# Performance work log

Hardware: AMD Instinct MI355X
Metric: run time of the kernel (lower is better)

## Reference

```python
import jax, jax.numpy as jnp
import numpy as np

EPS = 1e-5

def _ln(x, g, b):
    mu = jnp.mean(x, axis=-1, keepdims=True)
    var = jnp.mean(jnp.square(x - mu), axis=-1, keepdims=True)
    return (x - mu) * jax.lax.rsqrt(var + EPS) * g + b

def _gelu_new(x):
    # GPT-2 'gelu_new' (tanh approximation)
    c = jnp.asarray(np.sqrt(2.0 / np.pi), x.dtype)
    return 0.5 * x * (1.0 + jnp.tanh(c * (x + 0.044715 * x * x * x)))

def setup_inputs() -> dict:
    key = jax.random.key(0)
    ks = jax.random.split(key, 8)
    B, H, NH, HD, S = 16, 2048, 16, 128, 4096
    inv = lambda n: 1.0 / np.sqrt(n)
    return {
        "hidden_states": jax.random.normal(ks[0], (B, 1, H), jnp.float32),
        "cached_k": jax.random.normal(ks[1], (B, NH, S, HD), jnp.float32),
        "cached_v": jax.random.normal(ks[2], (B, NH, S, HD), jnp.float32),
        "ln1_g": jnp.ones((H,), jnp.float32),
        "ln1_b": jnp.zeros((H,), jnp.float32),
        "W_qkv": jax.random.normal(ks[3], (H, 3 * H), jnp.float32) * inv(H),
        "b_qkv": jnp.zeros((3 * H,), jnp.float32),
        "W_proj": jax.random.normal(ks[4], (H, H), jnp.float32) * inv(H),
        "b_proj": jnp.zeros((H,), jnp.float32),
        "ln2_g": jnp.ones((H,), jnp.float32),
        "ln2_b": jnp.zeros((H,), jnp.float32),
        "W_fc": jax.random.normal(ks[5], (H, 4 * H), jnp.float32) * inv(H),
        "b_fc": jnp.zeros((4 * H,), jnp.float32),
        "W_out": jax.random.normal(ks[6], (4 * H, H), jnp.float32) * inv(4 * H),
        "b_out": jnp.zeros((H,), jnp.float32),
    }

def reference(hidden_states, cached_k, cached_v, ln1_g, ln1_b, W_qkv, b_qkv,
              W_proj, b_proj, ln2_g, ln2_b, W_fc, b_fc, W_out, b_out):
    B, T, H = hidden_states.shape  # T == 1 (decode step)
    NH, HD = cached_k.shape[1], cached_k.shape[3]
    residual = hidden_states
    x = _ln(hidden_states, ln1_g, ln1_b)
    qkv = x @ W_qkv + b_qkv                        # [B,1,3H]
    q, k, v = jnp.split(qkv, 3, axis=-1)
    split = lambda t: t.reshape(B, T, NH, HD).transpose(0, 2, 1, 3)  # [B,NH,T,HD]
    q, k, v = split(q), split(k), split(v)
    k_full = jnp.concatenate([cached_k, k], axis=2)  # [B,NH,S+1,HD]
    v_full = jnp.concatenate([cached_v, v], axis=2)
    scale = 1.0 / jnp.sqrt(jnp.asarray(HD, q.dtype))
    scores = jnp.einsum('bhqd,bhkd->bhqk', q, k_full) * scale
    probs = jax.nn.softmax(scores, axis=-1)
    attn = jnp.einsum('bhqk,bhkd->bhqd', probs, v_full)  # [B,NH,1,HD]
    attn = attn.transpose(0, 2, 1, 3).reshape(B, T, H)
    attn = attn @ W_proj + b_proj
    h = attn + residual
    residual = h
    y = _ln(h, ln2_g, ln2_b)
    y = _gelu_new(y @ W_fc + b_fc) @ W_out + b_out
    return residual + y
```

## Files before the change

kernel.cpp:

```cpp
#include <hip/hip_runtime.h>
#include <hip/hip_bf16.h>

typedef unsigned int uint;


__global__ __launch_bounds__(256) void ln_f32_kernel(const float* __restrict__ in,
    const float* __restrict__ g, const float* __restrict__ bb, float* __restrict__ out)
{
    int row = blockIdx.x, t = threadIdx.x;
    const float* rp = in + row*2048;
    float4 a = ((const float4*)rp)[2*t];
    float4 b = ((const float4*)rp)[2*t+1];
    float v[8] = {a.x,a.y,a.z,a.w,b.x,b.y,b.z,b.w};
    float s=0.f, s2=0.f;
    #pragma unroll
    for(int i=0;i<8;i++){ s+=v[i]; s2+=v[i]*v[i]; }
    #pragma unroll
    for(int o=32;o>0;o>>=1){ s += __shfl_xor(s,o); s2 += __shfl_xor(s2,o); }
    __shared__ float red[8];
    int wv=t>>6, ln=t&63;
    if(ln==0){ red[wv]=s; red[4+wv]=s2; }
    __syncthreads();
    s  = red[0]+red[1]+red[2]+red[3];
    s2 = red[4]+red[5]+red[6]+red[7];
    float mu = s*(1.f/2048.f);
    float var = s2*(1.f/2048.f) - mu*mu;
    float rs = rsqrtf(var + 1e-5f);
    float4 g0 = ((const float4*)g)[2*t],  g1 = ((const float4*)g)[2*t+1];
    float4 b0 = ((const float4*)bb)[2*t], b1 = ((const float4*)bb)[2*t+1];
    float* op = out + row*2048 + t*8;
    float4 o0 = make_float4((v[0]-mu)*rs*g0.x+b0.x, (v[1]-mu)*rs*g0.y+b0.y,
                            (v[2]-mu)*rs*g0.z+b0.z, (v[3]-mu)*rs*g0.w+b0.w);
    float4 o1 = make_float4((v[4]-mu)*rs*g1.x+b1.x, (v[5]-mu)*rs*g1.y+b1.y,
                            (v[6]-mu)*rs*g1.z+b1.z, (v[7]-mu)*rs*g1.w+b1.w);
    ((float4*)op)[0]=o0; ((float4*)op)[1]=o1;
}

template<int KCHUNK>
__global__ __launch_bounds__(256) void gemm_sk(const float* __restrict__ X,
    const float* __restrict__ W, float* __restrict__ part, int K, int N, int colchunks)
{
    __shared__ float XS[16][KCHUNK];
    int cc = blockIdx.x % colchunks;
    int kc = blockIdx.x / colchunks;
    int k0 = kc * KCHUNK;
    for (int idx = threadIdx.x; idx < 16*KCHUNK; idx += 256){
        int m = idx / KCHUNK, i = idx % KCHUNK;
        XS[m][i] = X[m*K + k0 + i];
    }
    __syncthreads();
    int n0 = cc*512 + threadIdx.x*2;
    float a0[16], a1[16];
    #pragma unroll
    for(int m=0;m<16;m++){ a0[m]=0.f; a1[m]=0.f; }
    const float* Wp = W + (size_t)k0*N + n0;
    for (int i=0;i<KCHUNK;i+=4){
        float2 w0 = *(const float2*)(Wp + (size_t)(i+0)*N);
        float2 w1 = *(const float2*)(Wp + (size_t)(i+1)*N);
        float2 w2 = *(const float2*)(Wp + (size_t)(i+2)*N);
        float2 w3 = *(const float2*)(Wp + (size_t)(i+3)*N);
        #pragma unroll
        for(int m=0;m<16;m++){
            float4 x4 = *(const float4*)&XS[m][i];
            a0[m] += x4.x*w0.x + x4.y*w1.x + x4.z*w2.x + x4.w*w3.x;
            a1[m] += x4.x*w0.y + x4.y*w1.y + x4.z*w2.y + x4.w*w3.y;
        }
    }
    #pragma unroll
    for(int m=0;m<16;m++){
        *(float2*)&part[((size_t)(kc*16+m))*N + n0] = make_float2(a0[m], a1[m]);
    }
}

__global__ __launch_bounds__(256) void reduce_sk(const float* __restrict__ part, int N, int splitk,
    const float* __restrict__ bias, const float* __restrict__ res,
    float* __restrict__ outf, int mode)
{
    int n = blockIdx.x*256 + threadIdx.x;
    int m = blockIdx.y;
    size_t stride = (size_t)16*N;
    const float* p = part + (size_t)m*N + n;
    float s = 0.f;
    for (int kc=0;kc<splitk;kc++) s += p[(size_t)kc*stride];
    s += bias[n];
    if (mode==1 || mode==3) s += res[m*N+n];
    if (mode==2){
        float x = s;
        float t = tanhf(0.7978845608028654f*(x + 0.044715f*x*x*x));
        s = 0.5f*x*(1.f+t);
    }
    outf[m*N+n] = s;
}

__global__ __launch_bounds__(256, 8) void attn_chunk(const float* __restrict__ qkv,
    const float* __restrict__ Kc, const float* __restrict__ Vc, float* __restrict__ part)
{
    int h = blockIdx.y, b = blockIdx.z;
    int wave = threadIdx.x >> 6, lane = threadIdx.x & 63;
    int wc = blockIdx.x*4 + wave;
    int grp = lane >> 4, cl = lane & 15;
    const float* qrow = qkv + b*6144 + h*128 + cl*8;
    float4 qa = *(const float4*)qrow;
    float4 qb = *(const float4*)(qrow + 4);
    size_t bh = (size_t)(b*16+h);
    const float* Kbase = Kc + bh*4096*128;
    const float* Vbase = Vc + bh*4096*128;
    int jstart = wc * 128;
    float m = -1e30f, l = 0.f;
    float o[8];
    #pragma unroll
    for(int i=0;i<8;i++) o[i]=0.f;
    #pragma unroll 2
    for (int it=0; it<32; ++it){
        size_t off = (size_t)(jstart + it*4 + grp)*128 + cl*8;
        float4 ka = *(const float4*)(Kbase + off);
        float4 kb = *(const float4*)(Kbase + off + 4);
        float4 va = *(const float4*)(Vbase + off);
        float4 vb = *(const float4*)(Vbase + off + 4);
        float p = qa.x*ka.x + qa.y*ka.y + qa.z*ka.z + qa.w*ka.w
                + qb.x*kb.x + qb.y*kb.y + qb.z*kb.z + qb.w*kb.w;
        p += __shfl_xor(p,1); p += __shfl_xor(p,2);
        p += __shfl_xor(p,4); p += __shfl_xor(p,8);
        float sc = p * 0.08838834764831845f;
        float t = fmaxf(sc, __shfl_xor(sc,16));
        t = fmaxf(t, __shfl_xor(t,32));
        float mn = fmaxf(m, t);
        float f = __expf(m - mn);
        float e = __expf(sc - mn);
        l = l*f + e;
        o[0]=o[0]*f + e*va.x; o[1]=o[1]*f + e*va.y;
        o[2]=o[2]*f + e*va.z; o[3]=o[3]*f + e*va.w;
        o[4]=o[4]*f + e*vb.x; o[5]=o[5]*f + e*vb.y;
        o[6]=o[6]*f + e*vb.z; o[7]=o[7]*f + e*vb.w;
        m = mn;
    }
    if (wc == 31){
        const float* kn = qkv + b*6144 + 2048 + h*128 + cl*8;
        const float* vn = qkv + b*6144 + 4096 + h*128 + cl*8;
        float4 ka = *(const float4*)kn, kb = *(const float4*)(kn+4);
        float4 va = *(const float4*)vn, vb = *(const float4*)(vn+4);
        float p = qa.x*ka.x + qa.y*ka.y + qa.z*ka.z + qa.w*ka.w
                + qb.x*kb.x + qb.y*kb.y + qb.z*kb.z + qb.w*kb.w;
        p += __shfl_xor(p,1); p += __shfl_xor(p,2);
        p += __shfl_xor(p,4); p += __shfl_xor(p,8);
        float sc = p * 0.08838834764831845f;
        float mn = fmaxf(m, sc);
        float f = __expf(m - mn);
        float e = (grp==0) ? __expf(sc - mn) : 0.f;
        l = l*f + e;
        o[0]=o[0]*f + e*va.x; o[1]=o[1]*f + e*va.y;
        o[2]=o[2]*f + e*va.z; o[3]=o[3]*f + e*va.w;
        o[4]=o[4]*f + e*vb.x; o[5]=o[5]*f + e*vb.y;
        o[6]=o[6]*f + e*vb.z; o[7]=o[7]*f + e*vb.w;
        m = mn;
    }
    l += __shfl_xor(l,16); l += __shfl_xor(l,32);
    #pragma unroll
    for(int i=0;i<8;i++){ o[i] += __shfl_xor(o[i],16); o[i] += __shfl_xor(o[i],32); }
    float* pp = part + ((size_t)bh*32 + wc)*136;
    if (lane==0){ pp[0]=m; pp[1]=l; }
    if (lane<16){
        *(float4*)&pp[4 + lane*8]     = make_float4(o[0],o[1],o[2],o[3]);
        *(float4*)&pp[4 + lane*8 + 4] = make_float4(o[4],o[5],o[6],o[7]);
    }
}

__global__ __launch_bounds__(64) void attn_combine(const float* __restrict__ part,
                                                   float* __restrict__ attn_out)
{
    int bh = blockIdx.x;
    int lane = threadIdx.x;
    const float* pp = part + (size_t)bh*32*136;
    float M = -1e30f;
    for (int kc=0;kc<32;kc++) M = fmaxf(M, pp[kc*136]);
    float den=0.f, a0=0.f, a1=0.f;
    for (int kc=0;kc<32;kc++){
        float f = __expf(pp[kc*136] - M);
        den += f * pp[kc*136+1];
        float2 o = *(const float2*)&pp[kc*136 + 4 + 2*lane];
        a0 += f*o.x; a1 += f*o.y;
    }
    float inv = 1.f/den;
    int b = bh>>4, h = bh&15;
    float* op = attn_out + b*2048 + h*128 + 2*lane;
    op[0]=a0*inv; op[1]=a1*inv;
}

extern "C" void kernel_launch(void* const* d_in, const int* in_sizes, int n_in,
                              void* d_out, int out_size, void* d_ws, size_t ws_size,
                              hipStream_t stream)
{
    const float* hid  = (const float*)d_in[0];
    const float* Kc   = (const float*)d_in[1];
    const float* Vc   = (const float*)d_in[2];
    const float* ln1g = (const float*)d_in[3];
    const float* ln1b = (const float*)d_in[4];
    const float* Wqkv = (const float*)d_in[5];
    const float* bqkv = (const float*)d_in[6];
    const float* Wproj= (const float*)d_in[7];
    const float* bproj= (const float*)d_in[8];
    const float* ln2g = (const float*)d_in[9];
    const float* ln2b = (const float*)d_in[10];
    const float* Wfc  = (const float*)d_in[11];
    const float* bfc  = (const float*)d_in[12];
    const float* Wout = (const float*)d_in[13];
    const float* bout = (const float*)d_in[14];

    float* ws      = (float*)d_ws;
    float* xln     = ws;
    float* qkv     = xln + 32768;
    float* attn_o  = qkv + 98304;
    float* hbuf    = attn_o + 32768;
    float* yln     = hbuf + 32768;
    float* act     = yln + 32768;
    float* apart   = act + 131072;
    float* gpart   = apart + 1114112;

    ln_f32_kernel<<<16,256,0,stream>>>(hid, ln1g, ln1b, xln);
    gemm_sk<64><<<12*32,256,0,stream>>>(xln, Wqkv, gpart, 2048, 6144, 12);
    reduce_sk<<<dim3(24,16),256,0,stream>>>(gpart, 6144, 32, bqkv, nullptr, qkv, 0);
    attn_chunk<<<dim3(8,16,16),256,0,stream>>>(qkv, Kc, Vc, apart);
    attn_combine<<<256,64,0,stream>>>(apart, attn_o);
    gemm_sk<64><<<4*32,256,0,stream>>>(attn_o, Wproj, gpart, 2048, 2048, 4);
    reduce_sk<<<dim3(8,16),256,0,stream>>>(gpart, 2048, 32, bproj, hid, hbuf, 1);
    ln_f32_kernel<<<16,256,0,stream>>>(hbuf, ln2g, ln2b, yln);
    gemm_sk<64><<<16*32,256,0,stream>>>(yln, Wfc, gpart, 2048, 8192, 16);
    reduce_sk<<<dim3(32,16),256,0,stream>>>(gpart, 8192, 32, bfc, nullptr, act, 2);
    gemm_sk<128><<<4*64,256,0,stream>>>(act, Wout, gpart, 8192, 2048, 4);
    reduce_sk<<<dim3(8,16),256,0,stream>>>(gpart, 2048, 64, bout, hbuf, (float*)d_out, 3);
    (void)in_sizes; (void)n_in; (void)out_size; (void)ws_size;
}
```

Measured before the change: 399.8 us.

## Restructure attention chunk into two-pass score-then-value loop with full unroll

Replaces the per-step online softmax in attn_chunk with a two-pass scheme. All 32 K scores are computed into registers, a single max is taken, then one exp pass and a separate fully unrolled V accumulation follow. The aim is to expose many independent K and V loads at once for memory-level parallelism and to drop the per-step rescaling exps and serial dependency. It also removes the 8-blocks-per-CU launch bound, so register use rises and occupancy may fall.

After: 399.4 us (median of 2 runs). No clear change (-0.1%).

```diff
diff --git a/kernel.cpp b/kernel.cpp
--- a/kernel.cpp
+++ b/kernel.cpp
@@ -92,7 +92,7 @@
     outf[m*N+n] = s;
 }
 
-__global__ __launch_bounds__(256, 8) void attn_chunk(const float* __restrict__ qkv,
+__global__ __launch_bounds__(256) void attn_chunk(const float* __restrict__ qkv,
     const float* __restrict__ Kc, const float* __restrict__ Vc, float* __restrict__ part)
 {
     int h = blockIdx.y, b = blockIdx.z;
@@ -103,57 +103,65 @@
     float4 qa = *(const float4*)qrow;
     float4 qb = *(const float4*)(qrow + 4);
     size_t bh = (size_t)(b*16+h);
-    const float* Kbase = Kc + bh*4096*128;
-    const float* Vbase = Vc + bh*4096*128;
-    int jstart = wc * 128;
-    float m = -1e30f, l = 0.f;
-    float o[8];
-    #pragma unroll
-    for(int i=0;i<8;i++) o[i]=0.f;
-    #pragma unroll 2
-    for (int it=0; it<32; ++it){
-        size_t off = (size_t)(jstart + it*4 + grp)*128 + cl*8;
-        float4 ka = *(const float4*)(Kbase + off);
-        float4 kb = *(const float4*)(Kbase + off + 4);
-        float4 va = *(const float4*)(Vbase + off);
-        float4 vb = *(const float4*)(Vbase + off + 4);
+    size_t base = bh*524288 + (size_t)wc*16384 + (size_t)grp*128 + cl*8;
+    const float* Kp = Kc + base;
+    const float* Vp = Vc + base;
+
+    float s[32];
+    #pragma unroll
+    for (int i=0;i<32;i++){
+        const float* kp = Kp + (size_t)i*512;
+        float4 ka = *(const float4*)kp;
+        float4 kb = *(const float4*)(kp + 4);
         float p = qa.x*ka.x + qa.y*ka.y + qa.z*ka.z + qa.w*ka.w
                 + qb.x*kb.x + qb.y*kb.y + qb.z*kb.z + qb.w*kb.w;
         p += __shfl_xor(p,1); p += __shfl_xor(p,2);
         p += __shfl_xor(p,4); p += __shfl_xor(p,8);
-        float sc = p * 0.08838834764831845f;
-        float t = fmaxf(sc, __shfl_xor(sc,16));
-        t = fmaxf(t, __shfl_xor(t,32));
-        float mn = fmaxf(m, t);
-        float f = __expf(m - mn);
-        float e = __expf(sc - mn);
-        l = l*f + e;
-        o[0]=o[0]*f + e*va.x; o[1]=o[1]*f + e*va.y;
-        o[2]=o[2]*f + e*va.z; o[3]=o[3]*f + e*va.w;
-        o[4]=o[4]*f + e*vb.x; o[5]=o[5]*f + e*vb.y;
-        o[6]=o[6]*f + e*vb.z; o[7]=o[7]*f + e*vb.w;
-        m = mn;
-    }
+        s[i] = p * 0.08838834764831845f;
+    }
+    float m = s[0];
+    #pragma unroll
+    for (int i=1;i<32;i++) m = fmaxf(m, s[i]);
+    m = fmaxf(m, __shfl_xor(m,16));
+    m = fmaxf(m, __shfl_xor(m,32));
+
+    float sn = 0.f;
     if (wc == 31){
         const float* kn = qkv + b*6144 + 2048 + h*128 + cl*8;
-        const float* vn = qkv + b*6144 + 4096 + h*128 + cl*8;
         float4 ka = *(const float4*)kn, kb = *(const float4*)(kn+4);
-        float4 va = *(const float4*)vn, vb = *(const float4*)(vn+4);
         float p = qa.x*ka.x + qa.y*ka.y + qa.z*ka.z + qa.w*ka.w
                 + qb.x*kb.x + qb.y*kb.y + qb.z*kb.z + qb.w*kb.w;
         p += __shfl_xor(p,1); p += __shfl_xor(p,2);
         p += __shfl_xor(p,4); p += __shfl_xor(p,8);
-        float sc = p * 0.08838834764831845f;
-        float mn = fmaxf(m, sc);
-        float f = __expf(m - mn);
-        float e = (grp==0) ? __expf(sc - mn) : 0.f;
-        l = l*f + e;
-        o[0]=o[0]*f + e*va.x; o[1]=o[1]*f + e*va.y;
-        o[2]=o[2]*f + e*va.z; o[3]=o[3]*f + e*va.w;
-        o[4]=o[4]*f + e*vb.x; o[5]=o[5]*f + e*vb.y;
-        o[6]=o[6]*f + e*vb.z; o[7]=o[7]*f + e*vb.w;
-        m = mn;
-    }
+        sn = p * 0.08838834764831845f;
+        m = fmaxf(m, sn);
+    }
+
+    float l = 0.f;
+    #pragma unroll
+    for (int i=0;i<32;i++){ s[i] = __expf(s[i] - m); l += s[i]; }
+
+    float o[8];
+    #pragma unroll
+    for (int i=0;i<8;i++) o[i] = 0.f;
+    #pragma unroll
+    for (int i=0;i<32;i++){
+        const float* vp = Vp + (size_t)i*512;
+        float4 va = *(const float4*)vp;
+        float4 vb = *(const float4*)(vp + 4);
+        float e = s[i];
+        o[0]+=e*va.x; o[1]+=e*va.y; o[2]+=e*va.z; o[3]+=e*va.w;
+        o[4]+=e*vb.x; o[5]+=e*vb.y; o[6]+=e*vb.z; o[7]+=e*vb.w;
+    }
+    if (wc == 31){
+        const float* vn = qkv + b*6144 + 4096 + h*128 + cl*8;
+        float4 va = *(const float4*)vn, vb = *(const float4*)(vn+4);
+        float e = (grp==0) ? __expf(sn - m) : 0.f;
+        l += e;
+        o[0]+=e*va.x; o[1]+=e*va.y; o[2]+=e*va.z; o[3]+=e*va.w;
+        o[4]+=e*vb.x; o[5]+=e*vb.y; o[6]+=e*vb.z; o[7]+=e*vb.w;
+    }
+
     l += __shfl_xor(l,16); l += __shfl_xor(l,32);
     #pragma unroll
     for(int i=0;i<8;i++){ o[i] += __shfl_xor(o[i],16); o[i] += __shfl_xor(o[i],32); }
```
